# Performance work log

Hardware: AMD Instinct MI355X
Metric: run time of the kernel (lower is better)

Reference implementation:

```python
import jax, jax.numpy as jnp
import numpy as np

B = 524288
D = 128  # z_dim

def setup_inputs() -> dict:
    key = jax.random.key(0)
    kx, ky = jax.random.split(key)
    x = jax.random.normal(kx, (B, D), dtype=jnp.float32)
    y = jax.random.normal(ky, (B, D), dtype=jnp.float32)
    return {"x": x, "y": y}

def reference(x, y):
    # IQE-style quasimetric distance (QuasiMetric.get_distance)
    d = x.shape[-1]
    valid = x < y                                  # [B, D] bool
    xy = jnp.concatenate([x, y], axis=-1)          # [B, 2D]
    ixy = jnp.argsort(xy, axis=-1)                 # [B, 2D] indices
    sxy = jnp.take_along_axis(xy, ixy, axis=-1)    # sorted values
    sign = jnp.where(ixy < d, -1, 1)               # -1 for x entries, +1 for y
    neg_inc = jnp.take_along_axis(valid, ixy % d, axis=-1).astype(jnp.int32) * sign
    neg_cum = jnp.cumsum(neg_inc, axis=-1)
    neg_f = jnp.where(neg_cum < 0, -1.0, 0.0).astype(sxy.dtype)
    neg_incf = jnp.concatenate([neg_f[..., :1], jnp.diff(neg_f, axis=-1)], axis=-1)
    return (sxy * neg_incf).sum(-1)                # [B]
```

## Files before the change

### kernel.cpp

```cpp
#include <hip/hip_runtime.h>
#include <float.h>


constexpr int D = 128;
#define INF __builtin_huge_valf()

__device__ inline float med3(float a, float b, float c) {
    return __builtin_amdgcn_fmed3f(a, b, c);
}

template<int CTRL>
__device__ inline float dppmov(float v) {
    int i = __builtin_amdgcn_mov_dpp(__float_as_int(v), CTRL, 0xF, 0xF, true);
    return __int_as_float(i);
}
constexpr int QP_XOR1 = 0xB1;
constexpr int QP_XOR2 = 0x4E;
constexpr int QP_SHR1 = 0x90;

__device__ inline void cea(float& u, float& v) { float lo = fminf(u, v), hi = fmaxf(u, v); u = lo; v = hi; }
__device__ inline void ced(float& u, float& v) { float lo = fminf(u, v), hi = fmaxf(u, v); u = hi; v = lo; }
__device__ inline void cek(float& u, float& v, float s) {
    float lo = med3(u, v, s), hi = med3(u, v, -s); u = lo; v = hi;
}

template<int K, int J>
__device__ inline void sub_ct(float (&v)[32]) {
    #pragma unroll
    for (int r = 0; r < 32; r++)
        if (!(r & J)) { if (!(r & K)) cea(v[r], v[r + J]); else ced(v[r], v[r + J]); }
}
template<int J>
__device__ inline void sub_rt(float (&v)[32], float s) {
    #pragma unroll
    for (int r = 0; r < 32; r++)
        if (!(r & J)) cek(v[r], v[r + J], s);
}
template<int CTRL>
__device__ inline void cross(float (&v)[32], float sel) {
    #pragma unroll
    for (int r = 0; r < 32; r++) {
        float t = dppmov<CTRL>(v[r]);
        v[r] = med3(v[r], t, sel);
    }
}

__global__ __launch_bounds__(256) void iqe_union_kernel(
    const float* __restrict__ x, const float* __restrict__ y,
    float* __restrict__ out, int B)
{
    const int tid = threadIdx.x;
    const int g   = tid & 3;
    const int row = blockIdx.x * 64 + (tid >> 2);
    if (row >= B) return;

    const size_t rbase = (size_t)row * D;
    float a[32], b[32];
    #pragma unroll
    for (int t = 0; t < 8; t++) {
        *reinterpret_cast<float4*>(&a[4 * t]) = *reinterpret_cast<const float4*>(x + rbase + 16 * t + 4 * g);
        *reinterpret_cast<float4*>(&b[4 * t]) = *reinterpret_cast<const float4*>(y + rbase + 16 * t + 4 * g);
    }
    #pragma unroll
    for (int r = 0; r < 32; r++) {
        const bool v = a[r] < b[r];
        a[r] = v ? a[r] : FLT_MAX;
        b[r] = v ? b[r] : FLT_MAX;
    }

    const float S1 = (g & 1) ? 1.f : -1.f;
    const float S2 = (g & 2) ? 1.f : -1.f;
    const float M1 = S1 * INF;
    const float M2 = S2 * INF;
    const float C1 = -S1 * S2 * INF;

    sub_ct<2, 1>(a);  sub_ct<2, 1>(b);
    sub_ct<4, 2>(a);  sub_ct<4, 2>(b);
    sub_ct<4, 1>(a);  sub_ct<4, 1>(b);
    sub_ct<8, 4>(a);  sub_ct<8, 4>(b);
    sub_ct<8, 2>(a);  sub_ct<8, 2>(b);
    sub_ct<8, 1>(a);  sub_ct<8, 1>(b);
    sub_ct<16, 8>(a); sub_ct<16, 8>(b);
    sub_ct<16, 4>(a); sub_ct<16, 4>(b);
    sub_ct<16, 2>(a); sub_ct<16, 2>(b);
    sub_ct<16, 1>(a); sub_ct<16, 1>(b);
    sub_rt<16>(a, M1); sub_rt<16>(b, M1);
    sub_rt<8>(a, M1);  sub_rt<8>(b, M1);
    sub_rt<4>(a, M1);  sub_rt<4>(b, M1);
    sub_rt<2>(a, M1);  sub_rt<2>(b, M1);
    sub_rt<1>(a, M1);  sub_rt<1>(b, M1);
    cross<QP_XOR1>(a, C1); cross<QP_XOR1>(b, C1);
    sub_rt<16>(a, M2); sub_rt<16>(b, M2);
    sub_rt<8>(a, M2);  sub_rt<8>(b, M2);
    sub_rt<4>(a, M2);  sub_rt<4>(b, M2);
    sub_rt<2>(a, M2);  sub_rt<2>(b, M2);
    sub_rt<1>(a, M2);  sub_rt<1>(b, M2);
    cross<QP_XOR2>(a, M2); cross<QP_XOR2>(b, M2);
    cross<QP_XOR1>(a, M1); cross<QP_XOR1>(b, M1);
    sub_ct<128, 16>(a); sub_ct<128, 16>(b);
    sub_ct<128, 8>(a);  sub_ct<128, 8>(b);
    sub_ct<128, 4>(a);  sub_ct<128, 4>(b);
    sub_ct<128, 2>(a);  sub_ct<128, 2>(b);
    sub_ct<128, 1>(a);  sub_ct<128, 1>(b);

    float prev = dppmov<QP_SHR1>(b[31]);
    if (g == 0) prev = -FLT_MAX;
    float c = 0.f;
    #pragma unroll
    for (int r = 0; r < 32; r++) {
        c += fmaxf(0.f, b[r] - fmaxf(a[r], prev));
        prev = b[r];
    }
    c += dppmov<QP_XOR1>(c);
    c += dppmov<QP_XOR2>(c);
    if (g == 0) out[row] = c;
}

extern "C" void kernel_launch(void* const* d_in, const int* in_sizes, int n_in,
                              void* d_out, int out_size, void* d_ws, size_t ws_size,
                              hipStream_t stream) {
    const float* x = (const float*)d_in[0];
    const float* y = (const float*)d_in[1];
    float* out = (float*)d_out;
    const int B = in_sizes[0] / D;
    const int blocks = (B + 63) / 64;
    iqe_union_kernel<<<blocks, 256, 0, stream>>>(x, y, out, B);
}
```

Measured before the change: 523.8 us.

## Use persistent grid-stride loop with register prefetch of next row

Caps the grid at 2048 blocks and makes each block loop over rows with a grid stride. The next row's x and y values are loaded into a second set of registers while the current row is being sorted, so memory latency overlaps with the sorting network. The extra 64 floats of prefetch registers per thread raise register pressure and may lower occupancy or cause spills.

```diff
diff --git a/kernel.cpp b/kernel.cpp
--- a/kernel.cpp
+++ b/kernel.cpp
@@ -45,35 +45,8 @@
     }
 }
 
-__global__ __launch_bounds__(256) void iqe_union_kernel(
-    const float* __restrict__ x, const float* __restrict__ y,
-    float* __restrict__ out, int B)
-{
-    const int tid = threadIdx.x;
-    const int g   = tid & 3;
-    const int row = blockIdx.x * 64 + (tid >> 2);
-    if (row >= B) return;
-
-    const size_t rbase = (size_t)row * D;
-    float a[32], b[32];
-    #pragma unroll
-    for (int t = 0; t < 8; t++) {
-        *reinterpret_cast<float4*>(&a[4 * t]) = *reinterpret_cast<const float4*>(x + rbase + 16 * t + 4 * g);
-        *reinterpret_cast<float4*>(&b[4 * t]) = *reinterpret_cast<const float4*>(y + rbase + 16 * t + 4 * g);
-    }
-    #pragma unroll
-    for (int r = 0; r < 32; r++) {
-        const bool v = a[r] < b[r];
-        a[r] = v ? a[r] : FLT_MAX;
-        b[r] = v ? b[r] : FLT_MAX;
-    }
-
-    const float S1 = (g & 1) ? 1.f : -1.f;
-    const float S2 = (g & 2) ? 1.f : -1.f;
-    const float M1 = S1 * INF;
-    const float M2 = S2 * INF;
-    const float C1 = -S1 * S2 * INF;
-
+__device__ inline void sort128(float (&a)[32], float (&b)[32],
+                               float M1, float M2, float C1) {
     sub_ct<2, 1>(a);  sub_ct<2, 1>(b);
     sub_ct<4, 2>(a);  sub_ct<4, 2>(b);
     sub_ct<4, 1>(a);  sub_ct<4, 1>(b);
@@ -102,18 +75,70 @@
     sub_ct<128, 4>(a);  sub_ct<128, 4>(b);
     sub_ct<128, 2>(a);  sub_ct<128, 2>(b);
     sub_ct<128, 1>(a);  sub_ct<128, 1>(b);
+}
 
-    float prev = dppmov<QP_SHR1>(b[31]);
-    if (g == 0) prev = -FLT_MAX;
-    float c = 0.f;
-    #pragma unroll
-    for (int r = 0; r < 32; r++) {
-        c += fmaxf(0.f, b[r] - fmaxf(a[r], prev));
-        prev = b[r];
+__global__ __launch_bounds__(256) void iqe_union_kernel(
+    const float* __restrict__ x, const float* __restrict__ y,
+    float* __restrict__ out, int B)
+{
+    const int tid  = threadIdx.x;
+    const int g    = tid & 3;
+    const int lrow = tid >> 2;
+    const int rs   = (int)gridDim.x * 64;
+    int row = (int)blockIdx.x * 64 + lrow;
+
+    const float S1 = (g & 1) ? 1.f : -1.f;
+    const float S2 = (g & 2) ? 1.f : -1.f;
+    const float M1 = S1 * INF;
+    const float M2 = S2 * INF;
+    const float C1 = -S1 * S2 * INF;
+
+    float px[32], py[32];
+    if (row < B) {
+        const size_t rbase = (size_t)row * D;
+        #pragma unroll
+        for (int t = 0; t < 8; t++) {
+            *reinterpret_cast<float4*>(&px[4 * t]) = *reinterpret_cast<const float4*>(x + rbase + 16 * t + 4 * g);
+            *reinterpret_cast<float4*>(&py[4 * t]) = *reinterpret_cast<const float4*>(y + rbase + 16 * t + 4 * g);
+        }
     }
-    c += dppmov<QP_XOR1>(c);
-    c += dppmov<QP_XOR2>(c);
-    if (g == 0) out[row] = c;
+
+    for (; row < B; row += rs) {
+        float a[32], b[32];
+        #pragma unroll
+        for (int r = 0; r < 32; r++) { a[r] = px[r]; b[r] = py[r]; }
+
+        const int nrow = row + rs;
+        if (nrow < B) {
+            const size_t rbase = (size_t)nrow * D;
+            #pragma unroll
+            for (int t = 0; t < 8; t++) {
+                *reinterpret_cast<float4*>(&px[4 * t]) = *reinterpret_cast<const float4*>(x + rbase + 16 * t + 4 * g);
+                *reinterpret_cast<float4*>(&py[4 * t]) = *reinterpret_cast<const float4*>(y + rbase + 16 * t + 4 * g);
+            }
+        }
+
+        #pragma unroll
+        for (int r = 0; r < 32; r++) {
+            const bool v = a[r] < b[r];
+            a[r] = v ? a[r] : FLT_MAX;
+            b[r] = v ? b[r] : FLT_MAX;
+        }
+
+        sort128(a, b, M1, M2, C1);
+
+        float prev = dppmov<QP_SHR1>(b[31]);
+        if (g == 0) prev = -FLT_MAX;
+        float c = 0.f;
+        #pragma unroll
+        for (int r = 0; r < 32; r++) {
+            c += fmaxf(0.f, b[r] - fmaxf(a[r], prev));
+            prev = b[r];
+        }
+        c += dppmov<QP_XOR1>(c);
+        c += dppmov<QP_XOR2>(c);
+        if (g == 0) out[row] = c;
+    }
 }
 
 extern "C" void kernel_launch(void* const* d_in, const int* in_sizes, int n_in,
@@ -123,6 +148,7 @@
     const float* y = (const float*)d_in[1];
     float* out = (float*)d_out;
     const int B = in_sizes[0] / D;
-    const int blocks = (B + 63) / 64;
+    int blocks = (B + 63) / 64;
+    if (blocks > 2048) blocks = 2048;
     iqe_union_kernel<<<blocks, 256, 0, stream>>>(x, y, out, B);
 }
```

Result: no change. 532.6 us (+1.7%).

## Stream rows through LDS with async global_load_lds prefetch in persistent blocks

Applied to the files above, without the earlier changes.

Switches to a persistent grid of 512 blocks, each looping over chunks of 64 rows. Each wave prefetches the next chunk's x and y rows straight into LDS with global_load_lds while it sorts the current chunk in registers, so memory latency overlaps with the sorting network. Reads from LDS use a rotated index to reduce bank conflicts. In exchange the kernel uses 64KB of LDS per block, which limits occupancy, and each iteration waits on vmcnt(0).

```diff
diff --git a/kernel.cpp b/kernel.cpp
--- a/kernel.cpp
+++ b/kernel.cpp
@@ -1,5 +1,6 @@
 #include <hip/hip_runtime.h>
 #include <float.h>
+#include <stdint.h>
 
 
 constexpr int D = 128;
@@ -45,35 +46,8 @@
     }
 }
 
-__global__ __launch_bounds__(256) void iqe_union_kernel(
-    const float* __restrict__ x, const float* __restrict__ y,
-    float* __restrict__ out, int B)
-{
-    const int tid = threadIdx.x;
-    const int g   = tid & 3;
-    const int row = blockIdx.x * 64 + (tid >> 2);
-    if (row >= B) return;
-
-    const size_t rbase = (size_t)row * D;
-    float a[32], b[32];
-    #pragma unroll
-    for (int t = 0; t < 8; t++) {
-        *reinterpret_cast<float4*>(&a[4 * t]) = *reinterpret_cast<const float4*>(x + rbase + 16 * t + 4 * g);
-        *reinterpret_cast<float4*>(&b[4 * t]) = *reinterpret_cast<const float4*>(y + rbase + 16 * t + 4 * g);
-    }
-    #pragma unroll
-    for (int r = 0; r < 32; r++) {
-        const bool v = a[r] < b[r];
-        a[r] = v ? a[r] : FLT_MAX;
-        b[r] = v ? b[r] : FLT_MAX;
-    }
-
-    const float S1 = (g & 1) ? 1.f : -1.f;
-    const float S2 = (g & 2) ? 1.f : -1.f;
-    const float M1 = S1 * INF;
-    const float M2 = S2 * INF;
-    const float C1 = -S1 * S2 * INF;
-
+__device__ inline void sort128(float (&a)[32], float (&b)[32],
+                               float M1, float M2, float C1) {
     sub_ct<2, 1>(a);  sub_ct<2, 1>(b);
     sub_ct<4, 2>(a);  sub_ct<4, 2>(b);
     sub_ct<4, 1>(a);  sub_ct<4, 1>(b);
@@ -102,18 +76,88 @@
     sub_ct<128, 4>(a);  sub_ct<128, 4>(b);
     sub_ct<128, 2>(a);  sub_ct<128, 2>(b);
     sub_ct<128, 1>(a);  sub_ct<128, 1>(b);
+}
 
-    float prev = dppmov<QP_SHR1>(b[31]);
-    if (g == 0) prev = -FLT_MAX;
-    float c = 0.f;
-    #pragma unroll
-    for (int r = 0; r < 32; r++) {
-        c += fmaxf(0.f, b[r] - fmaxf(a[r], prev));
-        prev = b[r];
+__device__ inline void glds16(const float* g, float* l) {
+    __builtin_amdgcn_global_load_lds(
+        (const __attribute__((address_space(1))) void*)g,
+        (__attribute__((address_space(3))) void*)l, 16, 0, 0);
+}
+
+__global__ __launch_bounds__(256) void iqe_union_kernel(
+    const float* __restrict__ x, const float* __restrict__ y,
+    float* __restrict__ out, int B, int nch)
+{
+    __shared__ float lds[16384];
+    const int tid  = threadIdx.x;
+    const int lane = tid & 63;
+    const int wid  = tid >> 6;
+    const int g    = tid & 3;
+    const int lrow = (tid >> 2) & 15;
+    float* wbuf = &lds[wid * 4096];
+
+    const float S1 = (g & 1) ? 1.f : -1.f;
+    const float S2 = (g & 2) ? 1.f : -1.f;
+    const float M1 = S1 * INF;
+    const float M2 = S2 * INF;
+    const float C1 = -S1 * S2 * INF;
+
+    const int blockRow0 = blockIdx.x * nch * 64;
+
+    auto stage = [&](int c) {
+        const int r0 = blockRow0 + c * 64 + wid * 16;
+        if (r0 >= B) return;
+        const float* sx = x + (size_t)r0 * D + lane * 4;
+        const float* sy = y + (size_t)r0 * D + lane * 4;
+        #pragma unroll
+        for (int j = 0; j < 8; j++) glds16(sx + j * 256, wbuf + j * 256);
+        #pragma unroll
+        for (int j = 0; j < 8; j++) glds16(sy + j * 256, wbuf + 2048 + j * 256);
+    };
+
+    stage(0);
+
+    for (int c = 0; c < nch; c++) {
+        const int row = blockRow0 + c * 64 + wid * 16 + lrow;
+
+        asm volatile("s_waitcnt vmcnt(0)" ::: "memory");
+        __builtin_amdgcn_sched_barrier(0);
+
+        float a[32], b[32];
+        #pragma unroll
+        for (int t = 0; t < 8; t++) {
+            const int rd = (t + lrow) & 7;
+            *reinterpret_cast<float4*>(&a[4 * t]) =
+                *reinterpret_cast<const float4*>(wbuf + lrow * 128 + rd * 16 + g * 4);
+            *reinterpret_cast<float4*>(&b[4 * t]) =
+                *reinterpret_cast<const float4*>(wbuf + 2048 + lrow * 128 + rd * 16 + g * 4);
+        }
+
+        asm volatile("s_waitcnt lgkmcnt(0)" ::: "memory");
+        __builtin_amdgcn_sched_barrier(0);
+        if (c + 1 < nch) stage(c + 1);
+
+        #pragma unroll
+        for (int r = 0; r < 32; r++) {
+            const bool v = a[r] < b[r];
+            a[r] = v ? a[r] : FLT_MAX;
+            b[r] = v ? b[r] : FLT_MAX;
+        }
+
+        sort128(a, b, M1, M2, C1);
+
+        float prev = dppmov<QP_SHR1>(b[31]);
+        if (g == 0) prev = -FLT_MAX;
+        float acc = 0.f;
+        #pragma unroll
+        for (int r = 0; r < 32; r++) {
+            acc += fmaxf(0.f, b[r] - fmaxf(a[r], prev));
+            prev = b[r];
+        }
+        acc += dppmov<QP_XOR1>(acc);
+        acc += dppmov<QP_XOR2>(acc);
+        if (g == 0 && row < B) out[row] = acc;
     }
-    c += dppmov<QP_XOR1>(c);
-    c += dppmov<QP_XOR2>(c);
-    if (g == 0) out[row] = c;
 }
 
 extern "C" void kernel_launch(void* const* d_in, const int* in_sizes, int n_in,
@@ -123,6 +167,7 @@
     const float* y = (const float*)d_in[1];
     float* out = (float*)d_out;
     const int B = in_sizes[0] / D;
-    const int blocks = (B + 63) / 64;
-    iqe_union_kernel<<<blocks, 256, 0, stream>>>(x, y, out, B);
+    const int blocks = 512;
+    const int nch = (B + blocks * 64 - 1) / (blocks * 64);
+    iqe_union_kernel<<<blocks, 256, 0, stream>>>(x, y, out, B, nch);
 }
```

Result: slower. 546.1 us (+4.3%).

## Restructure sorting network with reflect/clean merges and split loads for overlap

Applied to the files above, without the earlier changes.

Swaps the bitonic network with alternating directions for a reflect-then-clean (flip) merge network. Each thread sorts two 16-element halves separately, then merges across registers and lanes using reversed DPP crosses (xor1, xor3). The loads are split into halves so sorting the first half can overlap the second-half memory latency. The aim is fewer med3 and compare operations and better latency hiding, at the cost of more temporary registers in the cross steps.

```diff
diff --git a/kernel.cpp b/kernel.cpp
--- a/kernel.cpp
+++ b/kernel.cpp
@@ -15,34 +15,63 @@
     return __int_as_float(i);
 }
 constexpr int QP_XOR1 = 0xB1;
-constexpr int QP_XOR2 = 0x4E;
+constexpr int QP_XOR3 = 0x1B;
 constexpr int QP_SHR1 = 0x90;
 
-__device__ inline void cea(float& u, float& v) { float lo = fminf(u, v), hi = fmaxf(u, v); u = lo; v = hi; }
-__device__ inline void ced(float& u, float& v) { float lo = fminf(u, v), hi = fmaxf(u, v); u = hi; v = lo; }
-__device__ inline void cek(float& u, float& v, float s) {
-    float lo = med3(u, v, s), hi = med3(u, v, -s); u = lo; v = hi;
+__device__ inline void cea(float& u, float& v) {
+    float lo = fminf(u, v), hi = fmaxf(u, v); u = lo; v = hi;
 }
 
-template<int K, int J>
-__device__ inline void sub_ct(float (&v)[32]) {
+template<int R0, int N, int J>
+__device__ inline void clean(float (&v)[32]) {
     #pragma unroll
-    for (int r = 0; r < 32; r++)
-        if (!(r & J)) { if (!(r & K)) cea(v[r], v[r + J]); else ced(v[r], v[r + J]); }
+    for (int i = 0; i < N; i++)
+        if (!(i & J)) cea(v[R0 + i], v[R0 + i + J]);
 }
-template<int J>
-__device__ inline void sub_rt(float (&v)[32], float s) {
+template<int R0, int N, int M>
+__device__ inline void reflect(float (&v)[32]) {
     #pragma unroll
-    for (int r = 0; r < 32; r++)
-        if (!(r & J)) cek(v[r], v[r + J], s);
+    for (int b = 0; b < N; b += M)
+        #pragma unroll
+        for (int i = 0; i < M / 2; i++)
+            cea(v[R0 + b + i], v[R0 + b + M - 1 - i]);
+}
+
+template<int R0>
+__device__ inline void sort16(float (&v)[32]) {
+    reflect<R0, 16, 2>(v);
+    reflect<R0, 16, 4>(v);  clean<R0, 16, 1>(v);
+    reflect<R0, 16, 8>(v);  clean<R0, 16, 2>(v); clean<R0, 16, 1>(v);
+    reflect<R0, 16, 16>(v); clean<R0, 16, 4>(v); clean<R0, 16, 2>(v); clean<R0, 16, 1>(v);
+}
+
+template<int CTRL>
+__device__ inline void cross_rev(float (&v)[32], float sel) {
+    float t[32];
+    #pragma unroll
+    for (int r = 0; r < 32; r++) t[r] = dppmov<CTRL>(v[31 - r]);
+    #pragma unroll
+    for (int r = 0; r < 32; r++) v[r] = med3(v[r], t[r], sel);
 }
 template<int CTRL>
-__device__ inline void cross(float (&v)[32], float sel) {
+__device__ inline void cross_same(float (&v)[32], float sel) {
+    float t[32];
     #pragma unroll
-    for (int r = 0; r < 32; r++) {
-        float t = dppmov<CTRL>(v[r]);
-        v[r] = med3(v[r], t, sel);
-    }
+    for (int r = 0; r < 32; r++) t[r] = dppmov<CTRL>(v[r]);
+    #pragma unroll
+    for (int r = 0; r < 32; r++) v[r] = med3(v[r], t[r], sel);
+}
+
+__device__ inline void merge_hi(float (&v)[32], float M1, float M2) {
+    reflect<0, 32, 32>(v);
+    clean<0, 32, 8>(v); clean<0, 32, 4>(v); clean<0, 32, 2>(v); clean<0, 32, 1>(v);
+    cross_rev<QP_XOR1>(v, M1);
+    clean<0, 32, 16>(v); clean<0, 32, 8>(v); clean<0, 32, 4>(v);
+    clean<0, 32, 2>(v);  clean<0, 32, 1>(v);
+    cross_rev<QP_XOR3>(v, M2);
+    cross_same<QP_XOR1>(v, M1);
+    clean<0, 32, 16>(v); clean<0, 32, 8>(v); clean<0, 32, 4>(v);
+    clean<0, 32, 2>(v);  clean<0, 32, 1>(v);
 }
 
 __global__ __launch_bounds__(256) void iqe_union_kernel(
@@ -57,51 +86,41 @@
     const size_t rbase = (size_t)row * D;
     float a[32], b[32];
     #pragma unroll
-    for (int t = 0; t < 8; t++) {
+    for (int t = 0; t < 4; t++)
         *reinterpret_cast<float4*>(&a[4 * t]) = *reinterpret_cast<const float4*>(x + rbase + 16 * t + 4 * g);
+    #pragma unroll
+    for (int t = 0; t < 4; t++)
         *reinterpret_cast<float4*>(&b[4 * t]) = *reinterpret_cast<const float4*>(y + rbase + 16 * t + 4 * g);
-    }
     #pragma unroll
-    for (int r = 0; r < 32; r++) {
-        const bool v = a[r] < b[r];
-        a[r] = v ? a[r] : FLT_MAX;
-        b[r] = v ? b[r] : FLT_MAX;
-    }
+    for (int t = 4; t < 8; t++)
+        *reinterpret_cast<float4*>(&a[4 * t]) = *reinterpret_cast<const float4*>(x + rbase + 16 * t + 4 * g);
+    #pragma unroll
+    for (int t = 4; t < 8; t++)
+        *reinterpret_cast<float4*>(&b[4 * t]) = *reinterpret_cast<const float4*>(y + rbase + 16 * t + 4 * g);
 
     const float S1 = (g & 1) ? 1.f : -1.f;
     const float S2 = (g & 2) ? 1.f : -1.f;
     const float M1 = S1 * INF;
     const float M2 = S2 * INF;
-    const float C1 = -S1 * S2 * INF;
 
-    sub_ct<2, 1>(a);  sub_ct<2, 1>(b);
-    sub_ct<4, 2>(a);  sub_ct<4, 2>(b);
-    sub_ct<4, 1>(a);  sub_ct<4, 1>(b);
-    sub_ct<8, 4>(a);  sub_ct<8, 4>(b);
-    sub_ct<8, 2>(a);  sub_ct<8, 2>(b);
-    sub_ct<8, 1>(a);  sub_ct<8, 1>(b);
-    sub_ct<16, 8>(a); sub_ct<16, 8>(b);
-    sub_ct<16, 4>(a); sub_ct<16, 4>(b);
-    sub_ct<16, 2>(a); sub_ct<16, 2>(b);
-    sub_ct<16, 1>(a); sub_ct<16, 1>(b);
-    sub_rt<16>(a, M1); sub_rt<16>(b, M1);
-    sub_rt<8>(a, M1);  sub_rt<8>(b, M1);
-    sub_rt<4>(a, M1);  sub_rt<4>(b, M1);
-    sub_rt<2>(a, M1);  sub_rt<2>(b, M1);
-    sub_rt<1>(a, M1);  sub_rt<1>(b, M1);
-    cross<QP_XOR1>(a, C1); cross<QP_XOR1>(b, C1);
-    sub_rt<16>(a, M2); sub_rt<16>(b, M2);
-    sub_rt<8>(a, M2);  sub_rt<8>(b, M2);
-    sub_rt<4>(a, M2);  sub_rt<4>(b, M2);
-    sub_rt<2>(a, M2);  sub_rt<2>(b, M2);
-    sub_rt<1>(a, M2);  sub_rt<1>(b, M2);
-    cross<QP_XOR2>(a, M2); cross<QP_XOR2>(b, M2);
-    cross<QP_XOR1>(a, M1); cross<QP_XOR1>(b, M1);
-    sub_ct<128, 16>(a); sub_ct<128, 16>(b);
-    sub_ct<128, 8>(a);  sub_ct<128, 8>(b);
-    sub_ct<128, 4>(a);  sub_ct<128, 4>(b);
-    sub_ct<128, 2>(a);  sub_ct<128, 2>(b);
-    sub_ct<128, 1>(a);  sub_ct<128, 1>(b);
+    #pragma unroll
+    for (int r = 0; r < 16; r++) {
+        const bool v = a[r] < b[r];
+        a[r] = v ? a[r] : FLT_MAX;
+        b[r] = v ? b[r] : FLT_MAX;
+    }
+    sort16<0>(a);  sort16<0>(b);
+
+    #pragma unroll
+    for (int r = 16; r < 32; r++) {
+        const bool v = a[r] < b[r];
+        a[r] = v ? a[r] : FLT_MAX;
+        b[r] = v ? b[r] : FLT_MAX;
+    }
+    sort16<16>(a); sort16<16>(b);
+
+    merge_hi(a, M1, M2);
+    merge_hi(b, M1, M2);
 
     float prev = dppmov<QP_SHR1>(b[31]);
     if (g == 0) prev = -FLT_MAX;
@@ -112,7 +131,7 @@
         prev = b[r];
     }
     c += dppmov<QP_XOR1>(c);
-    c += dppmov<QP_XOR2>(c);
+    c += dppmov<QP_XOR3>(c);
     if (g == 0) out[row] = c;
 }
 
```

After: 524.3 us. Within noise of the previous version (+0.1%).
